# Kernel tuning notes

Measured on AMD Instinct MI355X. Metric: run time of the kernel, lower is better.

The kernel has to match this reference:

```python
import jax, jax.numpy as jnp
import numpy as np

EMB = 1024
HEADS = 16
HEAD_DIM = EMB // HEADS
B, S = 4, 2048


def setup_inputs() -> dict:
    key = jax.random.key(0)
    ks = jax.random.split(key, 9)
    sc = 1.0 / np.sqrt(EMB)
    x = jax.random.normal(ks[0], (B, S, EMB), dtype=jnp.float32)
    Wq = jax.random.normal(ks[1], (EMB, EMB), dtype=jnp.float32) * sc
    bq = jax.random.normal(ks[2], (EMB,), dtype=jnp.float32) * 0.02
    Wk = jax.random.normal(ks[3], (EMB, EMB), dtype=jnp.float32) * sc
    bk = jax.random.normal(ks[4], (EMB,), dtype=jnp.float32) * 0.02
    Wv = jax.random.normal(ks[5], (EMB, EMB), dtype=jnp.float32) * sc
    bv = jax.random.normal(ks[6], (EMB,), dtype=jnp.float32) * 0.02
    Wo = jax.random.normal(ks[7], (EMB, EMB), dtype=jnp.float32) * sc
    bo = jax.random.normal(ks[8], (EMB,), dtype=jnp.float32) * 0.02
    # causal mask: 1 where allowed (lower triangular), 0 elsewhere
    causal_mask = jnp.tril(jnp.ones((S, S), dtype=jnp.int32))[None, None]
    return {"x": x, "Wq": Wq, "bq": bq, "Wk": Wk, "bk": bk,
            "Wv": Wv, "bv": bv, "Wo": Wo, "bo": bo,
            "causal_mask": causal_mask}


def reference(x, Wq, bq, Wk, bk, Wv, bv, Wo, bo, causal_mask):
    bs, seq, _ = x.shape
    # nn.Linear: x @ W.T + b; then view [bs, seq, H, hd] and transpose to [bs, H, seq, hd]
    def proj(W, b):
        return (x @ W.T + b).reshape(bs, seq, HEADS, HEAD_DIM).transpose(0, 2, 1, 3)
    q, k, v = proj(Wq, bq), proj(Wk, bk), proj(Wv, bv)
    scale = 1.0 / np.sqrt(HEAD_DIM).astype(np.float32)
    dots = jnp.einsum('bhqd,bhkd->bhqk', q, k) * scale  # [B, H, S, S]
    dots = jnp.where(causal_mask == 0, -jnp.inf, dots)
    attn = jax.nn.softmax(dots, axis=-1)
    out = jnp.einsum('bhqk,bhkd->bhqd', attn, v)  # [B, H, S, hd]
    out = out.transpose(0, 2, 1, 3).reshape(bs, seq, EMB)
    return out @ Wo.T + bo
```

## Files before the change

kernel.cpp:

```cpp
#include <hip/hip_runtime.h>
#include <hip/hip_bf16.h>

typedef __attribute__((ext_vector_type(8))) short short8;
typedef __attribute__((ext_vector_type(4))) float floatx4;

#define B_    4
#define S_    2048
#define EMB_  1024
#define NH_   16
#define HD_   64

#if __has_builtin(__builtin_amdgcn_exp2f)
#define EXP2F(x) __builtin_amdgcn_exp2f(x)
#else
#define EXP2F(x) exp2f(x)
#endif

__device__ __forceinline__ void async_cp16(const void* g, void* l) {
  __builtin_amdgcn_global_load_lds(
      (const __attribute__((address_space(1))) unsigned int*)g,
      (__attribute__((address_space(3))) unsigned int*)l, 16, 0, 0);
}

__device__ __forceinline__ ushort4 cvt4(const float4 f) {
  __bf16 t[4] = {(__bf16)f.x, (__bf16)f.y, (__bf16)f.z, (__bf16)f.w};
  return *(const ushort4*)t;
}

__global__ __launch_bounds__(256)
void cvt_kernel(const float* __restrict__ x,
                const float* __restrict__ wq, const float* __restrict__ wk,
                const float* __restrict__ wv, const float* __restrict__ wo,
                const float* __restrict__ bq, const float* __restrict__ bk,
                const float* __restrict__ bv,
                __bf16* __restrict__ xb, __bf16* __restrict__ Wcat,
                __bf16* __restrict__ Wob, float* __restrict__ bcat)
{
  const int NX4 = 2097152;
  const int NW4 = 262144;
  int g = blockIdx.x * 256 + threadIdx.x;
  if (g < NX4) {
    *(ushort4*)(xb + (size_t)g * 4) = cvt4(*(const float4*)(x + (size_t)g * 4));
    return;
  }
  g -= NX4;
  if (g < 3 * NW4) {
    const float* src = (g < NW4) ? wq : (g < 2 * NW4) ? wk : wv;
    const int gg = (g < NW4) ? g : (g < 2 * NW4) ? g - NW4 : g - 2 * NW4;
    *(ushort4*)(Wcat + (size_t)g * 4) = cvt4(*(const float4*)(src + (size_t)gg * 4));
    return;
  }
  g -= 3 * NW4;
  if (g < NW4) {
    *(ushort4*)(Wob + (size_t)g * 4) = cvt4(*(const float4*)(wo + (size_t)g * 4));
    return;
  }
  g -= NW4;
  if (g < 768) {
    const float* src = (g < 256) ? bq : (g < 512) ? bk : bv;
    *(float4*)(bcat + (size_t)g * 4) = *(const float4*)(src + (size_t)(g & 255) * 4);
  }
}

__global__ __launch_bounds__(256)
void gemm_qkv_kernel(const __bf16* __restrict__ A, const __bf16* __restrict__ W,
                     const float* __restrict__ bcat,
                     __bf16* __restrict__ Qb, __bf16* __restrict__ Kb,
                     __bf16* __restrict__ Vb)
{
  __shared__ __attribute__((aligned(16))) __bf16 As[128 * 32];
  __shared__ __attribute__((aligned(16))) __bf16 Ws[128 * 32];
  const int tid  = threadIdx.x;
  const int wave = tid >> 6, lane = tid & 63;
  const int l15  = lane & 15, quad = lane >> 4;
  const int wm   = wave >> 1, wn = wave & 1;
  const int bm   = blockIdx.y * 128;
  const int bn   = blockIdx.x * 128;
  const int widx = bn >> 10;
  const float QS = 0.180336880f;

  floatx4 acc[4][4];
#pragma unroll
  for (int i = 0; i < 4; ++i)
#pragma unroll
    for (int j = 0; j < 4; ++j) acc[i][j] = (floatx4){0.f, 0.f, 0.f, 0.f};

  const int srow = tid >> 2;
  const int scol = (tid & 3) << 3;
  const __bf16* Ag = A + (size_t)(bm + srow) * 1024 + scol;
  const __bf16* Wg = W + (size_t)(bn + srow) * 1024 + scol;
  __bf16* AsD = As + tid * 8;
  __bf16* WsD = Ws + tid * 8;

  for (int k0 = 0; k0 < 1024; k0 += 32) {
    __syncthreads();
    async_cp16(Ag + k0,             AsD);
    async_cp16(Ag + k0 + 64 * 1024, AsD + 2048);
    async_cp16(Wg + k0,             WsD);
    async_cp16(Wg + k0 + 64 * 1024, WsD + 2048);
    __syncthreads();
    short8 af[4], wf[4];
#pragma unroll
    for (int mi = 0; mi < 4; ++mi)
      af[mi] = *(const short8*)(As + ((wm * 64 + mi * 16 + l15) << 5) + (quad << 3));
#pragma unroll
    for (int ni = 0; ni < 4; ++ni)
      wf[ni] = *(const short8*)(Ws + ((wn * 64 + ni * 16 + l15) << 5) + (quad << 3));
#pragma unroll
    for (int mi = 0; mi < 4; ++mi)
#pragma unroll
      for (int ni = 0; ni < 4; ++ni)
        acc[mi][ni] = __builtin_amdgcn_mfma_f32_16x16x32_bf16(af[mi], wf[ni], acc[mi][ni], 0, 0, 0);
  }

#pragma unroll
  for (int ni = 0; ni < 4; ++ni) {
    const int n  = bn + wn * 64 + ni * 16 + l15;
    const float bvb = bcat[n];
    const int np = n & 1023;
    const int h = np >> 6, d = np & 63;
#pragma unroll
    for (int mi = 0; mi < 4; ++mi) {
      const int m0 = bm + wm * 64 + mi * 16 + quad * 4;
      const int b = m0 >> 11, s0 = m0 & 2047;
      floatx4 v = acc[mi][ni];
      if (widx == 0) {
        const size_t base = (size_t)(b * 16 + h) * (S_ * 64) + d;
#pragma unroll
        for (int r = 0; r < 4; ++r)
          Qb[base + (size_t)(s0 + r) * 64] = (__bf16)((v[r] + bvb) * QS);
      } else if (widx == 1) {
        const size_t base = (size_t)(b * 16 + h) * (S_ * 64) + d;
#pragma unroll
        for (int r = 0; r < 4; ++r)
          Kb[base + (size_t)(s0 + r) * 64] = (__bf16)(v[r] + bvb);
      } else {
        const size_t base = ((size_t)(b * 16 + h) * 64 + d) * S_ + s0;
        union { ushort4 u4; unsigned short u[4]; } pk;
#pragma unroll
        for (int r = 0; r < 4; ++r) {
          __bf16 hv = (__bf16)(v[r] + bvb);
          pk.u[r] = *(unsigned short*)&hv;
        }
        *(ushort4*)(Vb + base) = pk.u4;
      }
    }
  }
}

__device__ __forceinline__ void softmax_update(
    floatx4* s, float& mrun, float& lsum, floatx4* oacc,
    __bf16* psbase, const int l15, const int quad)
{
  float t0 = fmaxf(fmaxf(s[0][0], s[0][1]), fmaxf(s[0][2], s[0][3]));
  float t1 = fmaxf(fmaxf(s[1][0], s[1][1]), fmaxf(s[1][2], s[1][3]));
  float t2 = fmaxf(fmaxf(s[2][0], s[2][1]), fmaxf(s[2][2], s[2][3]));
  float t3 = fmaxf(fmaxf(s[3][0], s[3][1]), fmaxf(s[3][2], s[3][3]));
  float tmax = fmaxf(fmaxf(t0, t1), fmaxf(t2, t3));
  tmax = fmaxf(tmax, __shfl_xor(tmax, 16));
  tmax = fmaxf(tmax, __shfl_xor(tmax, 32));

  const float mold = mrun;
  if (!__all(tmax <= mold + 8.0f)) {
    const float mnew = fmaxf(mold, tmax);
    const float alpha = EXP2F(mold - mnew);
#pragma unroll
    for (int ni = 0; ni < 4; ++ni)
#pragma unroll
      for (int r = 0; r < 4; ++r) oacc[ni][r] *= alpha;
    lsum *= alpha;
    mrun = mnew;
  }
  const float m = mrun;
  float psum = 0.f;
#pragma unroll
  for (int ni = 0; ni < 4; ++ni) {
    float4 p;
    p.x = EXP2F(s[ni][0] - m);
    p.y = EXP2F(s[ni][1] - m);
    p.z = EXP2F(s[ni][2] - m);
    p.w = EXP2F(s[ni][3] - m);
    psum += (p.x + p.y) + (p.z + p.w);
    *(ushort4*)(psbase + l15 * 72 + ni * 16 + quad * 4) = cvt4(p);
  }
  lsum += psum;
}

__global__ __launch_bounds__(256, 2)
void attn_kernel(__bf16* __restrict__ Q, const __bf16* __restrict__ K,
                 const __bf16* __restrict__ Vt)
{
  __shared__ __attribute__((aligned(16))) __bf16 Ks[64 * 72];
  __shared__ __attribute__((aligned(16))) __bf16 Vs[64 * 72];
  __shared__ __attribute__((aligned(16))) __bf16 Ps[4][2][16 * 72];

  const int tid  = threadIdx.x;
  const int wave = tid >> 6, lane = tid & 63;
  const int l15  = lane & 15, quad = lane >> 4;
  const int qtA  = blockIdx.x, bh = blockIdx.y;
  const size_t hb = (size_t)bh * (S_ * 64);
  const float MASKV = -1.0e30f;

  const int srow = tid >> 3;
  const int scol = (tid & 7) << 3;

  for (int qsel = 0; qsel < 2; ++qsel) {
    const int qt = qsel ? (15 - qtA) : qtA;
    const int qw = qt * 128 + wave * 32;
    const int myqA = qw + l15;
    const int myqB = qw + 16 + l15;
    const int nsub = 2 * qt + 2;

    const __bf16* qpA = Q + hb + (size_t)myqA * 64 + quad * 8;
    const __bf16* qpB = Q + hb + (size_t)myqB * 64 + quad * 8;
    short8 aqA0 = *(const short8*)(qpA);
    short8 aqA1 = *(const short8*)(qpA + 32);
    short8 aqB0 = *(const short8*)(qpB);
    short8 aqB1 = *(const short8*)(qpB + 32);

    floatx4 oaccA[4], oaccB[4];
#pragma unroll
    for (int j = 0; j < 4; ++j) {
      oaccA[j] = (floatx4){0.f, 0.f, 0.f, 0.f};
      oaccB[j] = (floatx4){0.f, 0.f, 0.f, 0.f};
    }
    float lsumA = 0.f, lsumB = 0.f;
    float mrunA = MASKV, mrunB = MASKV;

    uint4 kreg0, kreg1, vreg0, vreg1;
    {
      const __bf16* kp = K  + hb + (size_t)srow * 64 + scol;
      const __bf16* vp = Vt + hb + (size_t)srow * S_ + scol;
      kreg0 = *(const uint4*)kp;
      kreg1 = *(const uint4*)(kp + 32 * 64);
      vreg0 = *(const uint4*)vp;
      vreg1 = *(const uint4*)(vp + (size_t)32 * S_);
    }

    for (int kt = 0; kt < nsub; ++kt) {
      __syncthreads();
      *(uint4*)(&Ks[srow * 72 + scol])        = kreg0;
      *(uint4*)(&Ks[(srow + 32) * 72 + scol]) = kreg1;
      *(uint4*)(&Vs[srow * 72 + scol])        = vreg0;
      *(uint4*)(&Vs[(srow + 32) * 72 + scol]) = vreg1;
      __syncthreads();

      if (kt + 1 < nsub) {
        const __bf16* kp = K  + hb + (size_t)((kt + 1) * 64 + srow) * 64 + scol;
        const __bf16* vp = Vt + hb + (size_t)srow * S_ + (kt + 1) * 64 + scol;
        kreg0 = *(const uint4*)kp;
        kreg1 = *(const uint4*)(kp + 32 * 64);
        vreg0 = *(const uint4*)vp;
        vreg1 = *(const uint4*)(vp + (size_t)32 * S_);
      }

      if (kt * 64 <= qw + 31) {
        floatx4 sA[4], sB[4];
#pragma unroll
        for (int j = 0; j < 4; ++j) {
          sA[j] = (floatx4){0.f, 0.f, 0.f, 0.f};
          sB[j] = (floatx4){0.f, 0.f, 0.f, 0.f};
        }
#pragma unroll
        for (int kk = 0; kk < 2; ++kk) {
          const short8 aqa = kk ? aqA1 : aqA0;
          const short8 aqb = kk ? aqB1 : aqB0;
          short8 bk[4];
#pragma unroll
          for (int ni = 0; ni < 4; ++ni)
            bk[ni] = *(const short8*)(&Ks[(ni * 16 + l15) * 72 + kk * 32 + quad * 8]);
#pragma unroll
          for (int ni = 0; ni < 4; ++ni)
            sA[ni] = __builtin_amdgcn_mfma_f32_16x16x32_bf16(bk[ni], aqa, sA[ni], 0, 0, 0);
#pragma unroll
          for (int ni = 0; ni < 4; ++ni)
            sB[ni] = __builtin_amdgcn_mfma_f32_16x16x32_bf16(bk[ni], aqb, sB[ni], 0, 0, 0);
        }

        const int kb = kt * 64 + quad * 4;
        if (kt * 64 + 63 > qw) {
#pragma unroll
          for (int ni = 0; ni < 4; ++ni)
#pragma unroll
            for (int r = 0; r < 4; ++r)
              if (kb + ni * 16 + r > myqA) sA[ni][r] = MASKV;
        }
        if (kt * 64 + 63 > qw + 16) {
#pragma unroll
          for (int ni = 0; ni < 4; ++ni)
#pragma unroll
            for (int r = 0; r < 4; ++r)
              if (kb + ni * 16 + r > myqB) sB[ni][r] = MASKV;
        }

        softmax_update(sA, mrunA, lsumA, oaccA, &Ps[wave][0][0], l15, quad);
        softmax_update(sB, mrunB, lsumB, oaccB, &Ps[wave][1][0], l15, quad);

        asm volatile("s_waitcnt lgkmcnt(0)" ::: "memory");
        __builtin_amdgcn_sched_barrier(0);

#pragma unroll
        for (int kk = 0; kk < 2; ++kk) {
          short8 bv[4];
#pragma unroll
          for (int ni = 0; ni < 4; ++ni)
            bv[ni] = *(const short8*)(&Vs[(ni * 16 + l15) * 72 + kk * 32 + quad * 8]);
          const short8 pfA = *(const short8*)(&Ps[wave][0][l15 * 72 + kk * 32 + quad * 8]);
          const short8 pfB = *(const short8*)(&Ps[wave][1][l15 * 72 + kk * 32 + quad * 8]);
#pragma unroll
          for (int ni = 0; ni < 4; ++ni)
            oaccA[ni] = __builtin_amdgcn_mfma_f32_16x16x32_bf16(bv[ni], pfA, oaccA[ni], 0, 0, 0);
#pragma unroll
          for (int ni = 0; ni < 4; ++ni)
            oaccB[ni] = __builtin_amdgcn_mfma_f32_16x16x32_bf16(bv[ni], pfB, oaccB[ni], 0, 0, 0);
        }
      }
    }

    {
      float l = lsumA;
      l += __shfl_xor(l, 16);
      l += __shfl_xor(l, 32);
      const float inv = 1.0f / fmaxf(l, 1e-20f);
      const size_t rowb = hb + (size_t)myqA * 64;
#pragma unroll
      for (int ni = 0; ni < 4; ++ni) {
        float4 o;
        o.x = oaccA[ni][0] * inv;
        o.y = oaccA[ni][1] * inv;
        o.z = oaccA[ni][2] * inv;
        o.w = oaccA[ni][3] * inv;
        *(ushort4*)(Q + rowb + ni * 16 + quad * 4) = cvt4(o);
      }
    }
    {
      float l = lsumB;
      l += __shfl_xor(l, 16);
      l += __shfl_xor(l, 32);
      const float inv = 1.0f / fmaxf(l, 1e-20f);
      const size_t rowb = hb + (size_t)myqB * 64;
#pragma unroll
      for (int ni = 0; ni < 4; ++ni) {
        float4 o;
        o.x = oaccB[ni][0] * inv;
        o.y = oaccB[ni][1] * inv;
        o.z = oaccB[ni][2] * inv;
        o.w = oaccB[ni][3] * inv;
        *(ushort4*)(Q + rowb + ni * 16 + quad * 4) = cvt4(o);
      }
    }
  }
}

__global__ __launch_bounds__(256)
void gemm_o_kernel(const __bf16* __restrict__ A, const __bf16* __restrict__ W,
                   const float* __restrict__ bias, float* __restrict__ out)
{
  __shared__ __attribute__((aligned(16))) __bf16 As[128 * 32];
  __shared__ __attribute__((aligned(16))) __bf16 Ws[128 * 32];
  const int tid  = threadIdx.x;
  const int wave = tid >> 6, lane = tid & 63;
  const int l15  = lane & 15, quad = lane >> 4;
  const int wm   = wave >> 1, wn = wave & 1;
  const int bm   = blockIdx.y * 128;
  const int bn   = blockIdx.x * 128;

  floatx4 acc[4][4];
#pragma unroll
  for (int i = 0; i < 4; ++i)
#pragma unroll
    for (int j = 0; j < 4; ++j) acc[i][j] = (floatx4){0.f, 0.f, 0.f, 0.f};

  const int srow = tid >> 2;
  const int scol = (tid & 3) << 3;
  const __bf16* Wg = W + (size_t)(bn + srow) * 1024 + scol;
  const int bb = bm >> 11;
  const int ss = (bm & 2047) + srow;
  __bf16* AsD = As + tid * 8;
  __bf16* WsD = Ws + tid * 8;

  for (int k0 = 0; k0 < 1024; k0 += 32) {
    const int c = k0 + scol, h = c >> 6, dd = c & 63;
    const __bf16* pa0 = A + (((size_t)(bb * 16 + h) * S_) + ss) * 64 + dd;
    __syncthreads();
    async_cp16(pa0,           AsD);
    async_cp16(pa0 + 64 * 64, AsD + 2048);
    async_cp16(Wg + k0,             WsD);
    async_cp16(Wg + k0 + 64 * 1024, WsD + 2048);
    __syncthreads();

    short8 af[4], wf[4];
#pragma unroll
    for (int mi = 0; mi < 4; ++mi)
      af[mi] = *(const short8*)(As + ((wm * 64 + mi * 16 + l15) << 5) + (quad << 3));
#pragma unroll
    for (int ni = 0; ni < 4; ++ni)
      wf[ni] = *(const short8*)(Ws + ((wn * 64 + ni * 16 + l15) << 5) + (quad << 3));
#pragma unroll
    for (int mi = 0; mi < 4; ++mi)
#pragma unroll
      for (int ni = 0; ni < 4; ++ni)
        acc[mi][ni] = __builtin_amdgcn_mfma_f32_16x16x32_bf16(af[mi], wf[ni], acc[mi][ni], 0, 0, 0);
  }

#pragma unroll
  for (int ni = 0; ni < 4; ++ni) {
    const int n = bn + wn * 64 + ni * 16 + l15;
    const float bvb = bias[n];
#pragma unroll
    for (int mi = 0; mi < 4; ++mi) {
      const int m0 = bm + wm * 64 + mi * 16 + quad * 4;
      floatx4 v = acc[mi][ni];
#pragma unroll
      for (int r = 0; r < 4; ++r)
        out[(size_t)(m0 + r) * 1024 + n] = v[r] + bvb;
    }
  }
}

extern "C" void kernel_launch(void* const* d_in, const int* in_sizes, int n_in,
                              void* d_out, int out_size, void* d_ws, size_t ws_size,
                              hipStream_t stream) {
  const float* x  = (const float*)d_in[0];
  const float* Wq = (const float*)d_in[1];
  const float* bq = (const float*)d_in[2];
  const float* Wk = (const float*)d_in[3];
  const float* bk = (const float*)d_in[4];
  const float* Wv = (const float*)d_in[5];
  const float* bv = (const float*)d_in[6];
  const float* Wo = (const float*)d_in[7];
  const float* bo = (const float*)d_in[8];

  const size_t BUF = (size_t)B_ * NH_ * S_ * HD_;
  __bf16* ws   = (__bf16*)d_ws;
  __bf16* xb   = ws;
  __bf16* Wcat = ws + 8388608;
  __bf16* Wob  = ws + 11534336;
  __bf16* Qb   = ws + 12582912;
  float*  bcat = (float*)(ws + 20971520);
  __bf16* Kb   = (__bf16*)d_out;
  __bf16* Vb   = (__bf16*)d_out + BUF;

  dim3 blk(256);
  cvt_kernel<<<12291, blk, 0, stream>>>(x, Wq, Wk, Wv, Wo, bq, bk, bv,
                                        xb, Wcat, Wob, bcat);
  gemm_qkv_kernel<<<dim3(24, 64), blk, 0, stream>>>(xb, Wcat, bcat, Qb, Kb, Vb);
  attn_kernel<<<dim3(8, 64), blk, 0, stream>>>(Qb, Kb, Vb);
  gemm_o_kernel<<<dim3(8, 64), blk, 0, stream>>>(Qb, Wob, bo, (float*)d_out);
}
```

Baseline: 274.9 us.

## Double-buffer K/V shared tiles and hoist V fragment loads before softmax

Switches the K and V LDS tiles to ping-pong buffers so the next tile is written to the alternate buffer while the current one is consumed, which cuts the two block barriers per iteration down to one. It also moves the V fragment reads from LDS ahead of the masking and softmax so their latency overlaps that ALU work. The cost is twice the K/V LDS footprint, which may limit occupancy with launch bounds of 2 blocks, and more live registers from the hoisted V fragments.

```diff
diff --git a/kernel.cpp b/kernel.cpp
--- a/kernel.cpp
+++ b/kernel.cpp
@@ -190,8 +190,8 @@
 void attn_kernel(__bf16* __restrict__ Q, const __bf16* __restrict__ K,
                  const __bf16* __restrict__ Vt)
 {
-  __shared__ __attribute__((aligned(16))) __bf16 Ks[64 * 72];
-  __shared__ __attribute__((aligned(16))) __bf16 Vs[64 * 72];
+  __shared__ __attribute__((aligned(16))) __bf16 Ks[2][64 * 72];
+  __shared__ __attribute__((aligned(16))) __bf16 Vs[2][64 * 72];
   __shared__ __attribute__((aligned(16))) __bf16 Ps[4][2][16 * 72];
 
   const int tid  = threadIdx.x;
@@ -236,22 +236,40 @@
       vreg0 = *(const uint4*)vp;
       vreg1 = *(const uint4*)(vp + (size_t)32 * S_);
     }
-
+    *(uint4*)(&Ks[0][srow * 72 + scol])        = kreg0;
+    *(uint4*)(&Ks[0][(srow + 32) * 72 + scol]) = kreg1;
+    *(uint4*)(&Vs[0][srow * 72 + scol])        = vreg0;
+    *(uint4*)(&Vs[0][(srow + 32) * 72 + scol]) = vreg1;
+    {
+      const __bf16* kp = K  + hb + (size_t)(64 + srow) * 64 + scol;
+      const __bf16* vp = Vt + hb + (size_t)srow * S_ + 64 + scol;
+      kreg0 = *(const uint4*)kp;
+      kreg1 = *(const uint4*)(kp + 32 * 64);
+      vreg0 = *(const uint4*)vp;
+      vreg1 = *(const uint4*)(vp + (size_t)32 * S_);
+    }
+    __syncthreads();
+
+    int p = 0;
     for (int kt = 0; kt < nsub; ++kt) {
-      __syncthreads();
-      *(uint4*)(&Ks[srow * 72 + scol])        = kreg0;
-      *(uint4*)(&Ks[(srow + 32) * 72 + scol]) = kreg1;
-      *(uint4*)(&Vs[srow * 72 + scol])        = vreg0;
-      *(uint4*)(&Vs[(srow + 32) * 72 + scol]) = vreg1;
-      __syncthreads();
+      __bf16* ksw = &Ks[p ^ 1][0];
+      __bf16* vsw = &Vs[p ^ 1][0];
+      const __bf16* ksr = &Ks[p][0];
+      const __bf16* vsr = &Vs[p][0];
 
       if (kt + 1 < nsub) {
-        const __bf16* kp = K  + hb + (size_t)((kt + 1) * 64 + srow) * 64 + scol;
-        const __bf16* vp = Vt + hb + (size_t)srow * S_ + (kt + 1) * 64 + scol;
-        kreg0 = *(const uint4*)kp;
-        kreg1 = *(const uint4*)(kp + 32 * 64);
-        vreg0 = *(const uint4*)vp;
-        vreg1 = *(const uint4*)(vp + (size_t)32 * S_);
+        *(uint4*)(&ksw[srow * 72 + scol])        = kreg0;
+        *(uint4*)(&ksw[(srow + 32) * 72 + scol]) = kreg1;
+        *(uint4*)(&vsw[srow * 72 + scol])        = vreg0;
+        *(uint4*)(&vsw[(srow + 32) * 72 + scol]) = vreg1;
+        if (kt + 2 < nsub) {
+          const __bf16* kp = K  + hb + (size_t)((kt + 2) * 64 + srow) * 64 + scol;
+          const __bf16* vp = Vt + hb + (size_t)srow * S_ + (kt + 2) * 64 + scol;
+          kreg0 = *(const uint4*)kp;
+          kreg1 = *(const uint4*)(kp + 32 * 64);
+          vreg0 = *(const uint4*)vp;
+          vreg1 = *(const uint4*)(vp + (size_t)32 * S_);
+        }
       }
 
       if (kt * 64 <= qw + 31) {
@@ -268,7 +286,7 @@
           short8 bk[4];
 #pragma unroll
           for (int ni = 0; ni < 4; ++ni)
-            bk[ni] = *(const short8*)(&Ks[(ni * 16 + l15) * 72 + kk * 32 + quad * 8]);
+            bk[ni] = *(const short8*)(&ksr[(ni * 16 + l15) * 72 + kk * 32 + quad * 8]);
 #pragma unroll
           for (int ni = 0; ni < 4; ++ni)
             sA[ni] = __builtin_amdgcn_mfma_f32_16x16x32_bf16(bk[ni], aqa, sA[ni], 0, 0, 0);
@@ -277,6 +295,15 @@
             sB[ni] = __builtin_amdgcn_mfma_f32_16x16x32_bf16(bk[ni], aqb, sB[ni], 0, 0, 0);
         }
 
+        const short8 v00 = *(const short8*)(&vsr[( 0 + l15) * 72 +      quad * 8]);
+        const short8 v01 = *(const short8*)(&vsr[(16 + l15) * 72 +      quad * 8]);
+        const short8 v02 = *(const short8*)(&vsr[(32 + l15) * 72 +      quad * 8]);
+        const short8 v03 = *(const short8*)(&vsr[(48 + l15) * 72 +      quad * 8]);
+        const short8 v10 = *(const short8*)(&vsr[( 0 + l15) * 72 + 32 + quad * 8]);
+        const short8 v11 = *(const short8*)(&vsr[(16 + l15) * 72 + 32 + quad * 8]);
+        const short8 v12 = *(const short8*)(&vsr[(32 + l15) * 72 + 32 + quad * 8]);
+        const short8 v13 = *(const short8*)(&vsr[(48 + l15) * 72 + 32 + quad * 8]);
+
         const int kb = kt * 64 + quad * 4;
         if (kt * 64 + 63 > qw) {
 #pragma unroll
@@ -299,22 +326,32 @@
         asm volatile("s_waitcnt lgkmcnt(0)" ::: "memory");
         __builtin_amdgcn_sched_barrier(0);
 
-#pragma unroll
-        for (int kk = 0; kk < 2; ++kk) {
-          short8 bv[4];
-#pragma unroll
-          for (int ni = 0; ni < 4; ++ni)
-            bv[ni] = *(const short8*)(&Vs[(ni * 16 + l15) * 72 + kk * 32 + quad * 8]);
-          const short8 pfA = *(const short8*)(&Ps[wave][0][l15 * 72 + kk * 32 + quad * 8]);
-          const short8 pfB = *(const short8*)(&Ps[wave][1][l15 * 72 + kk * 32 + quad * 8]);
-#pragma unroll
-          for (int ni = 0; ni < 4; ++ni)
-            oaccA[ni] = __builtin_amdgcn_mfma_f32_16x16x32_bf16(bv[ni], pfA, oaccA[ni], 0, 0, 0);
-#pragma unroll
-          for (int ni = 0; ni < 4; ++ni)
-            oaccB[ni] = __builtin_amdgcn_mfma_f32_16x16x32_bf16(bv[ni], pfB, oaccB[ni], 0, 0, 0);
+        {
+          const short8 pfA0 = *(const short8*)(&Ps[wave][0][l15 * 72 +      quad * 8]);
+          const short8 pfA1 = *(const short8*)(&Ps[wave][0][l15 * 72 + 32 + quad * 8]);
+          const short8 pfB0 = *(const short8*)(&Ps[wave][1][l15 * 72 +      quad * 8]);
+          const short8 pfB1 = *(const short8*)(&Ps[wave][1][l15 * 72 + 32 + quad * 8]);
+          oaccA[0] = __builtin_amdgcn_mfma_f32_16x16x32_bf16(v00, pfA0, oaccA[0], 0, 0, 0);
+          oaccA[1] = __builtin_amdgcn_mfma_f32_16x16x32_bf16(v01, pfA0, oaccA[1], 0, 0, 0);
+          oaccA[2] = __builtin_amdgcn_mfma_f32_16x16x32_bf16(v02, pfA0, oaccA[2], 0, 0, 0);
+          oaccA[3] = __builtin_amdgcn_mfma_f32_16x16x32_bf16(v03, pfA0, oaccA[3], 0, 0, 0);
+          oaccA[0] = __builtin_amdgcn_mfma_f32_16x16x32_bf16(v10, pfA1, oaccA[0], 0, 0, 0);
+          oaccA[1] = __builtin_amdgcn_mfma_f32_16x16x32_bf16(v11, pfA1, oaccA[1], 0, 0, 0);
+          oaccA[2] = __builtin_amdgcn_mfma_f32_16x16x32_bf16(v12, pfA1, oaccA[2], 0, 0, 0);
+          oaccA[3] = __builtin_amdgcn_mfma_f32_16x16x32_bf16(v13, pfA1, oaccA[3], 0, 0, 0);
+          oaccB[0] = __builtin_amdgcn_mfma_f32_16x16x32_bf16(v00, pfB0, oaccB[0], 0, 0, 0);
+          oaccB[1] = __builtin_amdgcn_mfma_f32_16x16x32_bf16(v01, pfB0, oaccB[1], 0, 0, 0);
+          oaccB[2] = __builtin_amdgcn_mfma_f32_16x16x32_bf16(v02, pfB0, oaccB[2], 0, 0, 0);
+          oaccB[3] = __builtin_amdgcn_mfma_f32_16x16x32_bf16(v03, pfB0, oaccB[3], 0, 0, 0);
+          oaccB[0] = __builtin_amdgcn_mfma_f32_16x16x32_bf16(v10, pfB1, oaccB[0], 0, 0, 0);
+          oaccB[1] = __builtin_amdgcn_mfma_f32_16x16x32_bf16(v11, pfB1, oaccB[1], 0, 0, 0);
+          oaccB[2] = __builtin_amdgcn_mfma_f32_16x16x32_bf16(v12, pfB1, oaccB[2], 0, 0, 0);
+          oaccB[3] = __builtin_amdgcn_mfma_f32_16x16x32_bf16(v13, pfB1, oaccB[3], 0, 0, 0);
         }
       }
+
+      __syncthreads();
+      p ^= 1;
     }
 
     {
```

Measured after the change: 284.3 us. 1.03x slower.

## Keep softmax probabilities in registers by permuting K rows to match MFMA operand layout

Applied to the files above, without the earlier changes.

The K rows read into shared memory are permuted so that the S accumulator layout coming out of the QK MFMA already matches the B-operand layout needed for the PV MFMA. The exponentiated probabilities are then packed straight into short8 registers instead of being written to and re-read from a per-wave LDS buffer. This drops that LDS round trip along with its waitcnt and sched barrier. The causal mask index math is updated to the permuted key order, and the K tile row stride changes from 72 to 80 elements, which alters the LDS bank pattern.

```diff
diff --git a/kernel.cpp b/kernel.cpp
--- a/kernel.cpp
+++ b/kernel.cpp
@@ -25,6 +25,13 @@
 __device__ __forceinline__ ushort4 cvt4(const float4 f) {
   __bf16 t[4] = {(__bf16)f.x, (__bf16)f.y, (__bf16)f.z, (__bf16)f.w};
   return *(const ushort4*)t;
+}
+
+__device__ __forceinline__ short8 pack8(const float4 a, const float4 b) {
+  union { short8 s; ushort4 u[2]; } r;
+  r.u[0] = cvt4(a);
+  r.u[1] = cvt4(b);
+  return r.s;
 }
 
 __global__ __launch_bounds__(256)
@@ -148,9 +155,9 @@
   }
 }
 
-__device__ __forceinline__ void softmax_update(
+__device__ __forceinline__ void softmax_update_pf(
     floatx4* s, float& mrun, float& lsum, floatx4* oacc,
-    __bf16* psbase, const int l15, const int quad)
+    short8& pf0, short8& pf1)
 {
   float t0 = fmaxf(fmaxf(s[0][0], s[0][1]), fmaxf(s[0][2], s[0][3]));
   float t1 = fmaxf(fmaxf(s[1][0], s[1][1]), fmaxf(s[1][2], s[1][3]));
@@ -172,27 +179,30 @@
     mrun = mnew;
   }
   const float m = mrun;
-  float psum = 0.f;
-#pragma unroll
-  for (int ni = 0; ni < 4; ++ni) {
-    float4 p;
-    p.x = EXP2F(s[ni][0] - m);
-    p.y = EXP2F(s[ni][1] - m);
-    p.z = EXP2F(s[ni][2] - m);
-    p.w = EXP2F(s[ni][3] - m);
-    psum += (p.x + p.y) + (p.z + p.w);
-    *(ushort4*)(psbase + l15 * 72 + ni * 16 + quad * 4) = cvt4(p);
-  }
-  lsum += psum;
+
+  float4 p0, p1, p2, p3;
+  p0.x = EXP2F(s[0][0] - m); p0.y = EXP2F(s[0][1] - m);
+  p0.z = EXP2F(s[0][2] - m); p0.w = EXP2F(s[0][3] - m);
+  p1.x = EXP2F(s[1][0] - m); p1.y = EXP2F(s[1][1] - m);
+  p1.z = EXP2F(s[1][2] - m); p1.w = EXP2F(s[1][3] - m);
+  p2.x = EXP2F(s[2][0] - m); p2.y = EXP2F(s[2][1] - m);
+  p2.z = EXP2F(s[2][2] - m); p2.w = EXP2F(s[2][3] - m);
+  p3.x = EXP2F(s[3][0] - m); p3.y = EXP2F(s[3][1] - m);
+  p3.z = EXP2F(s[3][2] - m); p3.w = EXP2F(s[3][3] - m);
+
+  lsum += ((p0.x + p0.y) + (p0.z + p0.w)) + ((p1.x + p1.y) + (p1.z + p1.w))
+        + ((p2.x + p2.y) + (p2.z + p2.w)) + ((p3.x + p3.y) + (p3.z + p3.w));
+
+  pf0 = pack8(p0, p2);
+  pf1 = pack8(p1, p3);
 }
 
 __global__ __launch_bounds__(256, 2)
 void attn_kernel(__bf16* __restrict__ Q, const __bf16* __restrict__ K,
                  const __bf16* __restrict__ Vt)
 {
-  __shared__ __attribute__((aligned(16))) __bf16 Ks[64 * 72];
+  __shared__ __attribute__((aligned(16))) __bf16 Ks[64 * 80];
   __shared__ __attribute__((aligned(16))) __bf16 Vs[64 * 72];
-  __shared__ __attribute__((aligned(16))) __bf16 Ps[4][2][16 * 72];
 
   const int tid  = threadIdx.x;
   const int wave = tid >> 6, lane = tid & 63;
@@ -203,6 +213,8 @@
 
   const int srow = tid >> 3;
   const int scol = (tid & 7) << 3;
+
+  const int rowbase = ((l15 >> 2) << 3) + (l15 & 3);
 
   for (int qsel = 0; qsel < 2; ++qsel) {
     const int qt = qsel ? (15 - qtA) : qtA;
@@ -239,8 +251,8 @@
 
     for (int kt = 0; kt < nsub; ++kt) {
       __syncthreads();
-      *(uint4*)(&Ks[srow * 72 + scol])        = kreg0;
-      *(uint4*)(&Ks[(srow + 32) * 72 + scol]) = kreg1;
+      *(uint4*)(&Ks[srow * 80 + scol])        = kreg0;
+      *(uint4*)(&Ks[(srow + 32) * 80 + scol]) = kreg1;
       *(uint4*)(&Vs[srow * 72 + scol])        = vreg0;
       *(uint4*)(&Vs[(srow + 32) * 72 + scol]) = vreg1;
       __syncthreads();
@@ -267,8 +279,10 @@
           const short8 aqb = kk ? aqB1 : aqB0;
           short8 bk[4];
 #pragma unroll
-          for (int ni = 0; ni < 4; ++ni)
-            bk[ni] = *(const short8*)(&Ks[(ni * 16 + l15) * 72 + kk * 32 + quad * 8]);
+          for (int ni = 0; ni < 4; ++ni) {
+            const int f = rowbase + ((ni & 1) << 5) + ((ni >> 1) << 2);
+            bk[ni] = *(const short8*)(&Ks[f * 80 + kk * 32 + quad * 8]);
+          }
 #pragma unroll
           for (int ni = 0; ni < 4; ++ni)
             sA[ni] = __builtin_amdgcn_mfma_f32_16x16x32_bf16(bk[ni], aqa, sA[ni], 0, 0, 0);
@@ -277,27 +291,29 @@
             sB[ni] = __builtin_amdgcn_mfma_f32_16x16x32_bf16(bk[ni], aqb, sB[ni], 0, 0, 0);
         }
 
-        const int kb = kt * 64 + quad * 4;
+        const int kb2 = kt * 64 + quad * 8;
         if (kt * 64 + 63 > qw) {
 #pragma unroll
           for (int ni = 0; ni < 4; ++ni)
 #pragma unroll
-            for (int r = 0; r < 4; ++r)
-              if (kb + ni * 16 + r > myqA) sA[ni][r] = MASKV;
+            for (int r = 0; r < 4; ++r) {
+              const int kvg = kb2 + ((ni & 1) << 5) + ((ni >> 1) << 2) + r;
+              if (kvg > myqA) sA[ni][r] = MASKV;
+            }
         }
         if (kt * 64 + 63 > qw + 16) {
 #pragma unroll
           for (int ni = 0; ni < 4; ++ni)
 #pragma unroll
-            for (int r = 0; r < 4; ++r)
-              if (kb + ni * 16 + r > myqB) sB[ni][r] = MASKV;
-        }
-
-        softmax_update(sA, mrunA, lsumA, oaccA, &Ps[wave][0][0], l15, quad);
-        softmax_update(sB, mrunB, lsumB, oaccB, &Ps[wave][1][0], l15, quad);
-
-        asm volatile("s_waitcnt lgkmcnt(0)" ::: "memory");
-        __builtin_amdgcn_sched_barrier(0);
+            for (int r = 0; r < 4; ++r) {
+              const int kvg = kb2 + ((ni & 1) << 5) + ((ni >> 1) << 2) + r;
+              if (kvg > myqB) sB[ni][r] = MASKV;
+            }
+        }
+
+        short8 pfA0, pfA1, pfB0, pfB1;
+        softmax_update_pf(sA, mrunA, lsumA, oaccA, pfA0, pfA1);
+        softmax_update_pf(sB, mrunB, lsumB, oaccB, pfB0, pfB1);
 
 #pragma unroll
         for (int kk = 0; kk < 2; ++kk) {
@@ -305,8 +321,8 @@
 #pragma unroll
           for (int ni = 0; ni < 4; ++ni)
             bv[ni] = *(const short8*)(&Vs[(ni * 16 + l15) * 72 + kk * 32 + quad * 8]);
-          const short8 pfA = *(const short8*)(&Ps[wave][0][l15 * 72 + kk * 32 + quad * 8]);
-          const short8 pfB = *(const short8*)(&Ps[wave][1][l15 * 72 + kk * 32 + quad * 8]);
+          const short8 pfA = kk ? pfA1 : pfA0;
+          const short8 pfB = kk ? pfB1 : pfB0;
 #pragma unroll
           for (int ni = 0; ni < 4; ++ni)
             oaccA[ni] = __builtin_amdgcn_mfma_f32_16x16x32_bf16(bv[ni], pfA, oaccA[ni], 0, 0, 0);
```

Measured after the change: 270.6 us. Within noise of the previous version (-1.6%).
